# Kernel optimization log

Measured on AMD Instinct MI355X. Metric: run time of the kernel, lower is better.

Reference implementation:

```python
import jax, jax.numpy as jnp
import numpy as np

SLOPE = 0.15  # LeakyReLU negative slope used throughout the module

def leaky(v):
    return jnp.where(v >= 0, v, SLOPE * v)

def _linear_params(key, fan_in, fan_out):
    kw, kb = jax.random.split(key)
    bound = 1.0 / np.sqrt(fan_in)
    W = jax.random.uniform(kw, (fan_in, fan_out), minval=-bound, maxval=bound, dtype=jnp.float32)
    b = jax.random.uniform(kb, (fan_out,), minval=-bound, maxval=bound, dtype=jnp.float32)
    return W, b

N_NODES = 50000
N_EDGES = 640000
IN_DIM = 128
EDGE_DIM = 64
HID = 128
LAT = 64

def setup_inputs() -> dict:
    key = jax.random.key(0)
    ks = jax.random.split(key, 12)
    x = jax.random.normal(ks[0], (N_NODES, IN_DIM), dtype=jnp.float32)
    edge_index = jax.random.randint(ks[1], (2, N_EDGES), 0, N_NODES, dtype=jnp.int32)
    edge_attr = jax.random.normal(ks[2], (N_EDGES, EDGE_DIM), dtype=jnp.float32)
    # conv1 params
    e1W1, e1b1 = _linear_params(ks[3], EDGE_DIM, HID)
    e1W2, e1b2 = _linear_params(ks[4], HID, HID)
    n1W, n1b = _linear_params(ks[5], IN_DIM + HID, HID)
    # conv2 params
    e2W1, e2b1 = _linear_params(ks[6], EDGE_DIM, HID)
    e2W2, e2b2 = _linear_params(ks[7], HID, HID)
    n2W, n2b = _linear_params(ks[8], HID + HID, HID)
    muW, mub = _linear_params(ks[9], HID, LAT)
    lvW, lvb = _linear_params(ks[10], HID, LAT)
    return {"x": x, "edge_index": edge_index, "edge_attr": edge_attr,
            "e1W1": e1W1, "e1b1": e1b1, "e1W2": e1W2, "e1b2": e1b2, "n1W": n1W, "n1b": n1b,
            "e2W1": e2W1, "e2b1": e2b1, "e2W2": e2W2, "e2b2": e2b2, "n2W": n2W, "n2b": n2b,
            "muW": muW, "mub": mub, "lvW": lvW, "lvb": lvb}

def edge_encoder(x, edge_index, edge_attr, eW1, eb1, eW2, eb2, nW, nb):
    # edge MLP: Linear -> LeakyReLU(0.15) -> Linear
    emb = leaky(edge_attr @ eW1 + eb1) @ eW2 + eb2           # [E, H]
    dst = edge_index[1]                                       # PyG x_i = x[target]
    z = jnp.concatenate([x[dst], emb], axis=1)                # [E, in+H]
    msg = z @ nW + nb                                         # [E, H]
    return jax.ops.segment_sum(msg, dst, num_segments=x.shape[0])  # aggr='add'

def reference(x, edge_index, edge_attr,
              e1W1, e1b1, e1W2, e1b2, n1W, n1b,
              e2W1, e2b1, e2W2, e2b2, n2W, n2b,
              muW, mub, lvW, lvb):
    # Dropout is identity in eval mode.
    h = leaky(edge_encoder(x, edge_index, edge_attr, e1W1, e1b1, e1W2, e1b2, n1W, n1b))
    h = leaky(edge_encoder(h, edge_index, edge_attr, e2W1, e2b1, e2W2, e2b2, n2W, n2b))
    mu = h @ muW + mub
    logvar = h @ lvW + lvb
    return (mu, logvar)
```

## Files before the change

kernel.cpp:

```cpp
#include <hip/hip_runtime.h>

typedef __bf16 bf16x4 __attribute__((ext_vector_type(4)));
typedef __bf16 bf16x8 __attribute__((ext_vector_type(8)));
typedef float  f32x4  __attribute__((ext_vector_type(4)));

constexpr int N_NODES = 50000;
constexpr int N_EDGES = 640000;
constexpr int NTILES  = 98;
constexpr int NB_EDGE = 2500;

__device__ __forceinline__ float leaky(float v) { return v >= 0.f ? v : 0.15f * v; }

__global__ void prep_kernel(
    const float* __restrict__ e1W1, const float* __restrict__ e1b1,
    const float* __restrict__ e1W2, const float* __restrict__ e1b2,
    const float* __restrict__ n1W,  const float* __restrict__ n1b,
    const float* __restrict__ e2W1, const float* __restrict__ e2b1,
    const float* __restrict__ e2W2, const float* __restrict__ e2b2,
    const float* __restrict__ n2W,  const float* __restrict__ n2b,
    const float* __restrict__ muW,  const float* __restrict__ mub,
    const float* __restrict__ lvW,  const float* __restrict__ lvb,
    __bf16* __restrict__ packE, __bf16* __restrict__ packN1,
    __bf16* __restrict__ packN2, __bf16* __restrict__ packH,
    float* __restrict__ ebias, float* __restrict__ c1, float* __restrict__ c2,
    float* __restrict__ hbias)
{
    int bid = blockIdx.x;
    int lane = threadIdx.x;
    int quad = lane >> 4, low = lane & 15;

    if (bid < 32) {
        int ct = bid >> 1, kt = bid & 1;
        for (int j = 0; j < 8; ++j) {
            int k = kt * 32 + quad * 8 + j;
            int n = ct * 16 + low;
            float v = (n < 128) ? e1W1[k * 128 + n] : e2W1[k * 128 + (n - 128)];
            packE[((ct * 2 + kt) * 64 + lane) * 8 + j] = (__bf16)v;
        }
    } else if (bid < 160) {
        bool is1 = bid < 96;
        int tile = bid - (is1 ? 32 : 96);
        const float* nW  = is1 ? n1W  : n2W;
        const float* eW2 = is1 ? e1W2 : e2W2;
        __bf16* dst = is1 ? packN1 : packN2;
        int ct = tile >> 3, kt = tile & 7;
        for (int j = 0; j < 8; ++j) {
            int k = kt * 32 + quad * 8 + j;
            int n = ct * 16 + low;
            float v;
            if (k < 128) {
                v = nW[k * 128 + n];
            } else {
                int i = k - 128;
                float acc = 0.f;
                for (int k2 = 0; k2 < 128; ++k2)
                    acc += eW2[i * 128 + k2] * nW[(128 + k2) * 128 + n];
                v = acc;
            }
            dst[((ct * 8 + kt) * 64 + lane) * 8 + j] = (__bf16)v;
        }
    } else if (bid < 192) {
        int tile = bid - 160;
        int ct = tile >> 2, kt = tile & 3;
        for (int j = 0; j < 8; ++j) {
            int k = kt * 32 + quad * 8 + j;
            int n = ct * 16 + low;
            float v = (n < 64) ? muW[k * 64 + n] : lvW[k * 64 + (n - 64)];
            packH[((ct * 4 + kt) * 64 + lane) * 8 + j] = (__bf16)v;
        }
    } else if (bid == 192 || bid == 193) {
        const float* nW  = (bid == 192) ? n1W  : n2W;
        const float* nb  = (bid == 192) ? n1b  : n2b;
        const float* eb2 = (bid == 192) ? e1b2 : e2b2;
        float* dst = (bid == 192) ? c1 : c2;
        for (int rep = 0; rep < 2; ++rep) {
            int j = lane + rep * 64;
            float acc = nb[j];
            for (int k = 0; k < 128; ++k)
                acc += eb2[k] * nW[(128 + k) * 128 + j];
            dst[j] = acc;
        }
    } else {
        for (int rep = 0; rep < 4; ++rep) {
            int j = lane + rep * 64;
            ebias[j] = (j < 128) ? e1b1[j] : e2b1[j - 128];
        }
        for (int rep = 0; rep < 2; ++rep) {
            int j = lane + rep * 64;
            hbias[j] = (j < 64) ? mub[j] : lvb[j - 64];
        }
    }
}

__global__ void hist_kernel(const int* __restrict__ dstp, int* __restrict__ deg) {
    int e = blockIdx.x * 256 + threadIdx.x;
    if (e < N_EDGES) atomicAdd(&deg[dstp[e]], 1);
}

__global__ void scan_a(const int* __restrict__ deg, int* __restrict__ offs,
                       int* __restrict__ tileSum, float* __restrict__ degf) {
    __shared__ int s[512];
    int t = threadIdx.x, i = blockIdx.x * 512 + t;
    int v = (i < N_NODES) ? deg[i] : 0;
    if (i < N_NODES) degf[i] = (float)v;
    s[t] = v; __syncthreads();
    for (int off = 1; off < 512; off <<= 1) {
        int x = (t >= off) ? s[t - off] : 0;
        __syncthreads();
        s[t] += x;
        __syncthreads();
    }
    if (i < N_NODES) offs[i] = s[t] - v;
    if (t == 511) tileSum[blockIdx.x] = s[511];
}

__global__ void scan_b(const int* __restrict__ tileSum, int* __restrict__ tileOff) {
    __shared__ int s[128];
    int t = threadIdx.x;
    int v = (t < NTILES) ? tileSum[t] : 0;
    s[t] = v; __syncthreads();
    for (int off = 1; off < 128; off <<= 1) {
        int x = (t >= off) ? s[t - off] : 0;
        __syncthreads();
        s[t] += x;
        __syncthreads();
    }
    if (t < NTILES) tileOff[t] = s[t] - v;
}

__global__ void scatter_kernel(const int* __restrict__ dstp, const int* __restrict__ offs,
                               const int* __restrict__ tileOff,
                               int* __restrict__ cursor, int* __restrict__ sorted,
                               int* __restrict__ sdst) {
    int e = blockIdx.x * 256 + threadIdx.x;
    if (e < N_EDGES) {
        int d = dstp[e];
        int p = offs[d] + tileOff[d >> 9] + atomicAdd(&cursor[d], 1);
        sorted[p] = e;
        sdst[p] = d;
    }
}

__global__ __launch_bounds__(256, 3) void edge_kernel(
    const float* __restrict__ edge_attr,
    const int* __restrict__ sorted, const int* __restrict__ sdst,
    const __bf16* __restrict__ packE,
    const float* __restrict__ ebias, float* __restrict__ S)
{
    __shared__ alignas(16) __bf16 Asd[2][64 * 64];
    __shared__ alignas(16) __bf16 Lball[4][64 * 64];

    int tid = threadIdx.x;
    int w = tid >> 6, lane = tid & 63;
    int quad = lane >> 4, low = lane & 15;
    int r = tid >> 2, c0 = (tid & 3) * 16;

    auto swz = [](int row, int cb) { return row * 128 + (cb ^ ((row & 7) << 4)); };

    bf16x8 bfragE[2][4];
    #pragma unroll
    for (int kt = 0; kt < 2; ++kt)
        #pragma unroll
        for (int ct = 0; ct < 4; ++ct)
            bfragE[kt][ct] = *reinterpret_cast<const bf16x8*>(
                packE + (((w * 4 + ct) * 2 + kt) * 64 + lane) * 8);
    float bias_c[4];
    #pragma unroll
    for (int ct = 0; ct < 4; ++ct) bias_c[ct] = ebias[w * 64 + ct * 16 + low];

    char* LbB = reinterpret_cast<char*>(&Lball[w][0]);

    constexpr int STRIDE = NB_EDGE * 64;
    int e0 = blockIdx.x * 64;

    auto stage = [&](int buf, const float4& a0, const float4& a1,
                     const float4& a2, const float4& a3) {
        char* AsB = reinterpret_cast<char*>(&Asd[buf][0]);
        bf16x8 v0, v1;
        v0[0]=(__bf16)a0.x; v0[1]=(__bf16)a0.y; v0[2]=(__bf16)a0.z; v0[3]=(__bf16)a0.w;
        v0[4]=(__bf16)a1.x; v0[5]=(__bf16)a1.y; v0[6]=(__bf16)a1.z; v0[7]=(__bf16)a1.w;
        v1[0]=(__bf16)a2.x; v1[1]=(__bf16)a2.y; v1[2]=(__bf16)a2.z; v1[3]=(__bf16)a2.w;
        v1[4]=(__bf16)a3.x; v1[5]=(__bf16)a3.y; v1[6]=(__bf16)a3.z; v1[7]=(__bf16)a3.w;
        *reinterpret_cast<bf16x8*>(AsB + swz(r, c0 * 2))      = v0;
        *reinterpret_cast<bf16x8*>(AsB + swz(r, c0 * 2 + 16)) = v1;
    };

    float4 f0, f1, f2, f3;
    int md_c, md_n, md_n2, ei_n2;
    {
        int ei = sorted[e0 + r];
        md_c = sdst[e0 + lane];
        const float4* ap = reinterpret_cast<const float4*>(edge_attr + (size_t)ei * 64 + c0);
        f0 = ap[0]; f1 = ap[1]; f2 = ap[2]; f3 = ap[3];
    }
    stage(0, f0, f1, f2, f3);
    {
        int ei1 = sorted[e0 + STRIDE + r];
        md_n = sdst[e0 + STRIDE + lane];
        const float4* ap = reinterpret_cast<const float4*>(edge_attr + (size_t)ei1 * 64 + c0);
        f0 = ap[0]; f1 = ap[1]; f2 = ap[2]; f3 = ap[3];
    }
    ei_n2 = sorted[e0 + 2 * STRIDE + r];
    md_n2 = sdst[e0 + 2 * STRIDE + lane];
    __syncthreads();
    int cur = 0;

    #pragma unroll 1
    for (int it = 0; it < 4; ++it) {
        if (it < 3) stage(cur ^ 1, f0, f1, f2, f3);

        float4 g0{}, g1{}, g2{}, g3{};
        if (it < 2) {
            const float4* gp = reinterpret_cast<const float4*>(
                edge_attr + (size_t)ei_n2 * 64 + c0);
            g0 = gp[0]; g1 = gp[1]; g2 = gp[2]; g3 = gp[3];
        }
        int ei_n3 = 0, md_n3 = 0;
        if (it < 1) {
            ei_n3 = sorted[e0 + 3 * STRIDE + r];
            md_n3 = sdst[e0 + 3 * STRIDE + lane];
        }

        int dp = __shfl_up(md_c, 1);
        bool flag = (lane > 0) && (md_c != dp);
        unsigned long long mask = __ballot(flag);
        int nruns = __popcll(mask) + 1;
        int rid = __popcll(mask & ((1ull << lane) - 1ull)) + (flag ? 1 : 0);
        int vdst = __builtin_amdgcn_ds_permute(rid << 2, md_c);

        const char* AsB = reinterpret_cast<const char*>(&Asd[cur][0]);
        f32x4 C1[4][4] = {};
        #pragma unroll
        for (int kt = 0; kt < 2; ++kt)
            #pragma unroll
            for (int rt = 0; rt < 4; ++rt) {
                bf16x8 a = *reinterpret_cast<const bf16x8*>(
                    AsB + swz(rt * 16 + low, kt * 64 + quad * 16));
                #pragma unroll
                for (int ct = 0; ct < 4; ++ct)
                    C1[rt][ct] = __builtin_amdgcn_mfma_f32_16x16x32_bf16(
                        a, bfragE[kt][ct], C1[rt][ct], 0, 0, 0);
            }

        #pragma unroll
        for (int rt = 0; rt < 4; ++rt)
            #pragma unroll
            for (int ct = 0; ct < 4; ++ct) {
                bf16x4 v;
                #pragma unroll
                for (int rr = 0; rr < 4; ++rr)
                    v[rr] = (__bf16)leaky(C1[rt][ct][rr] + bias_c[ct]);
                *reinterpret_cast<bf16x4*>(
                    LbB + swz(ct * 16 + low, rt * 32 + quad * 8)) = v;
            }

        for (int rt2 = 0; rt2 * 16 < nruns; ++rt2) {
            int target = rt2 * 16 + low;
            f32x4 C2[4] = {};
            #pragma unroll
            for (int kt = 0; kt < 2; ++kt) {
                int bsh = 63 - kt * 32 - quad * 8;
                bf16x8 a;
                #pragma unroll
                for (int j = 0; j < 8; ++j) {
                    int ride = __popcll(mask << (bsh - j));
                    a[j] = (ride == target) ? (__bf16)1.0f : (__bf16)0.0f;
                }
                #pragma unroll
                for (int ct = 0; ct < 4; ++ct) {
                    bf16x8 b = *reinterpret_cast<const bf16x8*>(
                        LbB + swz(ct * 16 + low, kt * 64 + quad * 16));
                    C2[ct] = __builtin_amdgcn_mfma_f32_16x16x32_bf16(a, b, C2[ct], 0, 0, 0);
                }
            }
            int node4[4];
            #pragma unroll
            for (int rr = 0; rr < 4; ++rr)
                node4[rr] = __shfl(vdst, rt2 * 16 + quad * 4 + rr);
            #pragma unroll
            for (int ct = 0; ct < 4; ++ct) {
                int col = w * 64 + ct * 16 + low;
                #pragma unroll
                for (int rr = 0; rr < 4; ++rr) {
                    int run = rt2 * 16 + quad * 4 + rr;
                    if (run < nruns && (unsigned)node4[rr] < (unsigned)N_NODES)
                        unsafeAtomicAdd(&S[(size_t)node4[rr] * 256 + col], C2[ct][rr]);
                }
            }
        }

        if (it < 3) __syncthreads();

        f0 = g0; f1 = g1; f2 = g2; f3 = g3;
        md_c = md_n; md_n = md_n2; md_n2 = md_n3; ei_n2 = ei_n3;
        cur ^= 1;
    }
}

__global__ __launch_bounds__(256) void node_fused(
    const float* __restrict__ x, const float* __restrict__ S,
    const float* __restrict__ degf,
    const __bf16* __restrict__ packN1, const __bf16* __restrict__ packN2,
    const __bf16* __restrict__ packH,
    const float* __restrict__ c1, const float* __restrict__ c2,
    const float* __restrict__ hbias,
    float* __restrict__ out)
{
    constexpr int HS = 152;
    __shared__ __bf16 Hs[4][16 * HS];
    int w = threadIdx.x >> 6, lane = threadIdx.x & 63;
    int quad = lane >> 4, low = lane & 15;
    int rb = blockIdx.x * 64 + w * 16;

    int arow = rb + low;
    if (arow >= N_NODES) arow = N_NODES - 1;
    float ds = degf[arow];
    const float* xrow = x + (size_t)arow * 128;
    const float* Srow = S + (size_t)arow * 256;

    float deg4[4];
    #pragma unroll
    for (int rr = 0; rr < 4; ++rr) {
        int row = rb + quad * 4 + rr;
        deg4[rr] = degf[row < N_NODES ? row : N_NODES - 1];
    }

    __bf16* Hw = Hs[w];

    f32x4 C[8] = {};
    #pragma unroll
    for (int kt = 0; kt < 8; ++kt) {
        const float* base = (kt < 4) ? (xrow + kt * 32 + quad * 8)
                                     : (Srow + (kt - 4) * 32 + quad * 8);
        float4 p0 = *reinterpret_cast<const float4*>(base);
        float4 p1 = *reinterpret_cast<const float4*>(base + 4);
        float m = (kt < 4) ? ds : 1.f;
        bf16x8 a;
        a[0]=(__bf16)(p0.x*m); a[1]=(__bf16)(p0.y*m); a[2]=(__bf16)(p0.z*m); a[3]=(__bf16)(p0.w*m);
        a[4]=(__bf16)(p1.x*m); a[5]=(__bf16)(p1.y*m); a[6]=(__bf16)(p1.z*m); a[7]=(__bf16)(p1.w*m);
        #pragma unroll
        for (int ct = 0; ct < 8; ++ct) {
            bf16x8 b = *reinterpret_cast<const bf16x8*>(packN1 + ((ct * 8 + kt) * 64 + lane) * 8);
            C[ct] = __builtin_amdgcn_mfma_f32_16x16x32_bf16(a, b, C[ct], 0, 0, 0);
        }
    }
    #pragma unroll
    for (int ct = 0; ct < 8; ++ct) {
        int col = ct * 16 + low;
        float cb = c1[col];
        #pragma unroll
        for (int rr = 0; rr < 4; ++rr) {
            float v = leaky(C[ct][rr] + deg4[rr] * cb);
            Hw[(quad * 4 + rr) * HS + col] = (__bf16)(v * deg4[rr]);
        }
    }

    f32x4 C2[8] = {};
    #pragma unroll
    for (int kt = 0; kt < 8; ++kt) {
        bf16x8 a;
        if (kt < 4) {
            a = *reinterpret_cast<const bf16x8*>(&Hw[low * HS + kt * 32 + quad * 8]);
        } else {
            const float* base = Srow + 128 + (kt - 4) * 32 + quad * 8;
            float4 p0 = *reinterpret_cast<const float4*>(base);
            float4 p1 = *reinterpret_cast<const float4*>(base + 4);
            a[0]=(__bf16)p0.x; a[1]=(__bf16)p0.y; a[2]=(__bf16)p0.z; a[3]=(__bf16)p0.w;
            a[4]=(__bf16)p1.x; a[5]=(__bf16)p1.y; a[6]=(__bf16)p1.z; a[7]=(__bf16)p1.w;
        }
        #pragma unroll
        for (int ct = 0; ct < 8; ++ct) {
            bf16x8 b = *reinterpret_cast<const bf16x8*>(packN2 + ((ct * 8 + kt) * 64 + lane) * 8);
            C2[ct] = __builtin_amdgcn_mfma_f32_16x16x32_bf16(a, b, C2[ct], 0, 0, 0);
        }
    }
    #pragma unroll
    for (int ct = 0; ct < 8; ++ct) {
        int col = ct * 16 + low;
        float cb = c2[col];
        #pragma unroll
        for (int rr = 0; rr < 4; ++rr) {
            float v = leaky(C2[ct][rr] + deg4[rr] * cb);
            Hw[(quad * 4 + rr) * HS + col] = (__bf16)v;
        }
    }

    f32x4 C3[8] = {};
    #pragma unroll
    for (int kt = 0; kt < 4; ++kt) {
        bf16x8 a = *reinterpret_cast<const bf16x8*>(&Hw[low * HS + kt * 32 + quad * 8]);
        #pragma unroll
        for (int ct = 0; ct < 8; ++ct) {
            bf16x8 b = *reinterpret_cast<const bf16x8*>(packH + ((ct * 4 + kt) * 64 + lane) * 8);
            C3[ct] = __builtin_amdgcn_mfma_f32_16x16x32_bf16(a, b, C3[ct], 0, 0, 0);
        }
    }
    #pragma unroll
    for (int ct = 0; ct < 8; ++ct) {
        int col = ct * 16 + low;
        float hb = hbias[col];
        #pragma unroll
        for (int rr = 0; rr < 4; ++rr) {
            int row = rb + quad * 4 + rr;
            if (row >= N_NODES) continue;
            float v = C3[ct][rr] + hb;
            if (col < 64) out[(size_t)row * 64 + col] = v;
            else          out[(size_t)N_NODES * 64 + (size_t)row * 64 + (col - 64)] = v;
        }
    }
}

extern "C" void kernel_launch(void* const* d_in, const int* in_sizes, int n_in,
                              void* d_out, int out_size, void* d_ws, size_t ws_size,
                              hipStream_t stream)
{
    const float* x     = (const float*)d_in[0];
    const int*   eidx  = (const int*)  d_in[1];
    const float* eattr = (const float*)d_in[2];
    const float* e1W1 = (const float*)d_in[3];
    const float* e1b1 = (const float*)d_in[4];
    const float* e1W2 = (const float*)d_in[5];
    const float* e1b2 = (const float*)d_in[6];
    const float* n1W  = (const float*)d_in[7];
    const float* n1b  = (const float*)d_in[8];
    const float* e2W1 = (const float*)d_in[9];
    const float* e2b1 = (const float*)d_in[10];
    const float* e2W2 = (const float*)d_in[11];
    const float* e2b2 = (const float*)d_in[12];
    const float* n2W  = (const float*)d_in[13];
    const float* n2b  = (const float*)d_in[14];
    const float* muW  = (const float*)d_in[15];
    const float* mub  = (const float*)d_in[16];
    const float* lvW  = (const float*)d_in[17];
    const float* lvb  = (const float*)d_in[18];

    const int* dstp = eidx + N_EDGES;

    char* ws = (char*)d_ws;
    size_t off = 0;
    auto alloc = [&](size_t bytes) -> void* {
        void* p = ws + off;
        off = (off + bytes + 1023) & ~(size_t)1023;
        return p;
    };
    float* S       = (float*)alloc((size_t)N_NODES * 256 * 4);
    float* h       = (float*)alloc((size_t)N_NODES * 128 * 4);
    float* g       = (float*)alloc((size_t)N_NODES * 128 * 4);
    int*   deg     = (int*)  alloc((size_t)N_NODES * 4);
    int*   cursor  = (int*)  alloc((size_t)N_NODES * 4);
    int*   offs    = (int*)  alloc((size_t)N_NODES * 4);
    float* degf    = (float*)alloc((size_t)N_NODES * 4);
    int*   sorted  = (int*)  alloc((size_t)N_EDGES * 4);
    int*   tileSum = (int*)  alloc(NTILES * 4);
    int*   tileOff = (int*)  alloc(NTILES * 4);
    __bf16* packE  = (__bf16*)alloc(32 * 64 * 8 * 2);
    __bf16* packN1 = (__bf16*)alloc(64 * 64 * 8 * 2);
    __bf16* packN2 = (__bf16*)alloc(64 * 64 * 8 * 2);
    __bf16* packH  = (__bf16*)alloc(32 * 64 * 8 * 2);
    float* ebias   = (float*)alloc(256 * 4);
    float* c1      = (float*)alloc(128 * 4);
    float* c2      = (float*)alloc(128 * 4);
    float* hbias   = (float*)alloc(128 * 4);
    (void)ws_size; (void)in_sizes; (void)n_in; (void)out_size; (void)h;

    int* sdst = (int*)g;

    hipMemsetAsync(S, 0, (size_t)N_NODES * 256 * 4, stream);
    hipMemsetAsync(deg, 0, 2 * (((size_t)N_NODES * 4 + 1023) & ~(size_t)1023), stream);

    prep_kernel<<<195, 64, 0, stream>>>(e1W1, e1b1, e1W2, e1b2, n1W, n1b,
                                        e2W1, e2b1, e2W2, e2b2, n2W, n2b,
                                        muW, mub, lvW, lvb,
                                        packE, packN1, packN2, packH,
                                        ebias, c1, c2, hbias);

    hist_kernel<<<N_EDGES / 256, 256, 0, stream>>>(dstp, deg);
    scan_a<<<NTILES, 512, 0, stream>>>(deg, offs, tileSum, degf);
    scan_b<<<1, 128, 0, stream>>>(tileSum, tileOff);
    scatter_kernel<<<N_EDGES / 256, 256, 0, stream>>>(dstp, offs, tileOff, cursor, sorted, sdst);

    edge_kernel<<<NB_EDGE, 256, 0, stream>>>(eattr, sorted, sdst, packE, ebias, S);

    node_fused<<<(N_NODES + 63) / 64, 256, 0, stream>>>(
        x, S, degf, packN1, packN2, packH, c1, c2, hbias, (float*)d_out);
}
```

Measured before the change: 527.5 us.

## Replace persistent pipelined edge kernel with one 64-edge tile per block

```diff
diff --git a/kernel.cpp b/kernel.cpp
--- a/kernel.cpp
+++ b/kernel.cpp
@@ -7,7 +7,6 @@
 constexpr int N_NODES = 50000;
 constexpr int N_EDGES = 640000;
 constexpr int NTILES  = 98;
-constexpr int NB_EDGE = 2500;
 
 __device__ __forceinline__ float leaky(float v) { return v >= 0.f ? v : 0.15f * v; }
 
@@ -141,13 +140,13 @@
     }
 }
 
-__global__ __launch_bounds__(256, 3) void edge_kernel(
+__global__ __launch_bounds__(256, 4) void edge_kernel(
     const float* __restrict__ edge_attr,
     const int* __restrict__ sorted, const int* __restrict__ sdst,
     const __bf16* __restrict__ packE,
     const float* __restrict__ ebias, float* __restrict__ S)
 {
-    __shared__ alignas(16) __bf16 Asd[2][64 * 64];
+    __shared__ alignas(16) __bf16 As[64 * 64];
     __shared__ alignas(16) __bf16 Lball[4][64 * 64];
 
     int tid = threadIdx.x;
@@ -157,143 +156,99 @@
 
     auto swz = [](int row, int cb) { return row * 128 + (cb ^ ((row & 7) << 4)); };
 
-    bf16x8 bfragE[2][4];
-    #pragma unroll
-    for (int kt = 0; kt < 2; ++kt)
-        #pragma unroll
-        for (int ct = 0; ct < 4; ++ct)
-            bfragE[kt][ct] = *reinterpret_cast<const bf16x8*>(
-                packE + (((w * 4 + ct) * 2 + kt) * 64 + lane) * 8);
+    char* AsB = reinterpret_cast<char*>(As);
+    char* LbB = reinterpret_cast<char*>(&Lball[w][0]);
+
+    int e0 = blockIdx.x * 64;
+
+    int ei = sorted[e0 + r];
+    int md = sdst[e0 + lane];
+    const float4* ap = reinterpret_cast<const float4*>(edge_attr + (size_t)ei * 64 + c0);
+    float4 f0 = ap[0], f1 = ap[1], f2 = ap[2], f3 = ap[3];
+
+    int dp = __shfl_up(md, 1);
+    bool flag = (lane > 0) && (md != dp);
+    unsigned long long mask = __ballot(flag);
+    int nruns = __popcll(mask) + 1;
+    int rid = __popcll(mask & ((1ull << lane) - 1ull)) + (flag ? 1 : 0);
+    int vdst = __builtin_amdgcn_ds_permute(rid << 2, md);
+
     float bias_c[4];
     #pragma unroll
     for (int ct = 0; ct < 4; ++ct) bias_c[ct] = ebias[w * 64 + ct * 16 + low];
 
-    char* LbB = reinterpret_cast<char*>(&Lball[w][0]);
-
-    constexpr int STRIDE = NB_EDGE * 64;
-    int e0 = blockIdx.x * 64;
-
-    auto stage = [&](int buf, const float4& a0, const float4& a1,
-                     const float4& a2, const float4& a3) {
-        char* AsB = reinterpret_cast<char*>(&Asd[buf][0]);
+    {
         bf16x8 v0, v1;
-        v0[0]=(__bf16)a0.x; v0[1]=(__bf16)a0.y; v0[2]=(__bf16)a0.z; v0[3]=(__bf16)a0.w;
-        v0[4]=(__bf16)a1.x; v0[5]=(__bf16)a1.y; v0[6]=(__bf16)a1.z; v0[7]=(__bf16)a1.w;
-        v1[0]=(__bf16)a2.x; v1[1]=(__bf16)a2.y; v1[2]=(__bf16)a2.z; v1[3]=(__bf16)a2.w;
-        v1[4]=(__bf16)a3.x; v1[5]=(__bf16)a3.y; v1[6]=(__bf16)a3.z; v1[7]=(__bf16)a3.w;
+        v0[0]=(__bf16)f0.x; v0[1]=(__bf16)f0.y; v0[2]=(__bf16)f0.z; v0[3]=(__bf16)f0.w;
+        v0[4]=(__bf16)f1.x; v0[5]=(__bf16)f1.y; v0[6]=(__bf16)f1.z; v0[7]=(__bf16)f1.w;
+        v1[0]=(__bf16)f2.x; v1[1]=(__bf16)f2.y; v1[2]=(__bf16)f2.z; v1[3]=(__bf16)f2.w;
+        v1[4]=(__bf16)f3.x; v1[5]=(__bf16)f3.y; v1[6]=(__bf16)f3.z; v1[7]=(__bf16)f3.w;
         *reinterpret_cast<bf16x8*>(AsB + swz(r, c0 * 2))      = v0;
         *reinterpret_cast<bf16x8*>(AsB + swz(r, c0 * 2 + 16)) = v1;
-    };
-
-    float4 f0, f1, f2, f3;
-    int md_c, md_n, md_n2, ei_n2;
-    {
-        int ei = sorted[e0 + r];
-        md_c = sdst[e0 + lane];
-        const float4* ap = reinterpret_cast<const float4*>(edge_attr + (size_t)ei * 64 + c0);
-        f0 = ap[0]; f1 = ap[1]; f2 = ap[2]; f3 = ap[3];
-    }
-    stage(0, f0, f1, f2, f3);
-    {
-        int ei1 = sorted[e0 + STRIDE + r];
-        md_n = sdst[e0 + STRIDE + lane];
-        const float4* ap = reinterpret_cast<const float4*>(edge_attr + (size_t)ei1 * 64 + c0);
-        f0 = ap[0]; f1 = ap[1]; f2 = ap[2]; f3 = ap[3];
-    }
-    ei_n2 = sorted[e0 + 2 * STRIDE + r];
-    md_n2 = sdst[e0 + 2 * STRIDE + lane];
+    }
     __syncthreads();
-    int cur = 0;
-
-    #pragma unroll 1
-    for (int it = 0; it < 4; ++it) {
-        if (it < 3) stage(cur ^ 1, f0, f1, f2, f3);
-
-        float4 g0{}, g1{}, g2{}, g3{};
-        if (it < 2) {
-            const float4* gp = reinterpret_cast<const float4*>(
-                edge_attr + (size_t)ei_n2 * 64 + c0);
-            g0 = gp[0]; g1 = gp[1]; g2 = gp[2]; g3 = gp[3];
-        }
-        int ei_n3 = 0, md_n3 = 0;
-        if (it < 1) {
-            ei_n3 = sorted[e0 + 3 * STRIDE + r];
-            md_n3 = sdst[e0 + 3 * STRIDE + lane];
-        }
-
-        int dp = __shfl_up(md_c, 1);
-        bool flag = (lane > 0) && (md_c != dp);
-        unsigned long long mask = __ballot(flag);
-        int nruns = __popcll(mask) + 1;
-        int rid = __popcll(mask & ((1ull << lane) - 1ull)) + (flag ? 1 : 0);
-        int vdst = __builtin_amdgcn_ds_permute(rid << 2, md_c);
-
-        const char* AsB = reinterpret_cast<const char*>(&Asd[cur][0]);
-        f32x4 C1[4][4] = {};
-        #pragma unroll
-        for (int kt = 0; kt < 2; ++kt)
-            #pragma unroll
-            for (int rt = 0; rt < 4; ++rt) {
-                bf16x8 a = *reinterpret_cast<const bf16x8*>(
-                    AsB + swz(rt * 16 + low, kt * 64 + quad * 16));
-                #pragma unroll
-                for (int ct = 0; ct < 4; ++ct)
-                    C1[rt][ct] = __builtin_amdgcn_mfma_f32_16x16x32_bf16(
-                        a, bfragE[kt][ct], C1[rt][ct], 0, 0, 0);
-            }
-
-        #pragma unroll
-        for (int rt = 0; rt < 4; ++rt)
+
+    f32x4 C1[4][4] = {};
+    #pragma unroll
+    for (int kt = 0; kt < 2; ++kt)
+        #pragma unroll
+        for (int rt = 0; rt < 4; ++rt) {
+            bf16x8 a = *reinterpret_cast<const bf16x8*>(
+                AsB + swz(rt * 16 + low, kt * 64 + quad * 16));
             #pragma unroll
             for (int ct = 0; ct < 4; ++ct) {
-                bf16x4 v;
-                #pragma unroll
-                for (int rr = 0; rr < 4; ++rr)
-                    v[rr] = (__bf16)leaky(C1[rt][ct][rr] + bias_c[ct]);
-                *reinterpret_cast<bf16x4*>(
-                    LbB + swz(ct * 16 + low, rt * 32 + quad * 8)) = v;
+                bf16x8 b = *reinterpret_cast<const bf16x8*>(
+                    packE + (((w * 4 + ct) * 2 + kt) * 64 + lane) * 8);
+                C1[rt][ct] = __builtin_amdgcn_mfma_f32_16x16x32_bf16(
+                    a, b, C1[rt][ct], 0, 0, 0);
             }
-
-        for (int rt2 = 0; rt2 * 16 < nruns; ++rt2) {
-            int target = rt2 * 16 + low;
-            f32x4 C2[4] = {};
-            #pragma unroll
-            for (int kt = 0; kt < 2; ++kt) {
-                int bsh = 63 - kt * 32 - quad * 8;
-                bf16x8 a;
-                #pragma unroll
-                for (int j = 0; j < 8; ++j) {
-                    int ride = __popcll(mask << (bsh - j));
-                    a[j] = (ride == target) ? (__bf16)1.0f : (__bf16)0.0f;
-                }
-                #pragma unroll
-                for (int ct = 0; ct < 4; ++ct) {
-                    bf16x8 b = *reinterpret_cast<const bf16x8*>(
-                        LbB + swz(ct * 16 + low, kt * 64 + quad * 16));
-                    C2[ct] = __builtin_amdgcn_mfma_f32_16x16x32_bf16(a, b, C2[ct], 0, 0, 0);
-                }
-            }
-            int node4[4];
+        }
+
+    #pragma unroll
+    for (int rt = 0; rt < 4; ++rt)
+        #pragma unroll
+        for (int ct = 0; ct < 4; ++ct) {
+            bf16x4 v;
             #pragma unroll
             for (int rr = 0; rr < 4; ++rr)
-                node4[rr] = __shfl(vdst, rt2 * 16 + quad * 4 + rr);
+                v[rr] = (__bf16)leaky(C1[rt][ct][rr] + bias_c[ct]);
+            *reinterpret_cast<bf16x4*>(
+                LbB + swz(ct * 16 + low, rt * 32 + quad * 8)) = v;
+        }
+
+    for (int rt2 = 0; rt2 * 16 < nruns; ++rt2) {
+        int target = rt2 * 16 + low;
+        f32x4 C2[4] = {};
+        #pragma unroll
+        for (int kt = 0; kt < 2; ++kt) {
+            int bsh = 63 - kt * 32 - quad * 8;
+            bf16x8 a;
+            #pragma unroll
+            for (int j = 0; j < 8; ++j) {
+                int ride = __popcll(mask << (bsh - j));
+                a[j] = (ride == target) ? (__bf16)1.0f : (__bf16)0.0f;
+            }
             #pragma unroll
             for (int ct = 0; ct < 4; ++ct) {
-                int col = w * 64 + ct * 16 + low;
-                #pragma unroll
-                for (int rr = 0; rr < 4; ++rr) {
-                    int run = rt2 * 16 + quad * 4 + rr;
-                    if (run < nruns && (unsigned)node4[rr] < (unsigned)N_NODES)
-                        unsafeAtomicAdd(&S[(size_t)node4[rr] * 256 + col], C2[ct][rr]);
-                }
+                bf16x8 b = *reinterpret_cast<const bf16x8*>(
+                    LbB + swz(ct * 16 + low, kt * 64 + quad * 16));
+                C2[ct] = __builtin_amdgcn_mfma_f32_16x16x32_bf16(a, b, C2[ct], 0, 0, 0);
             }
         }
-
-        if (it < 3) __syncthreads();
-
-        f0 = g0; f1 = g1; f2 = g2; f3 = g3;
-        md_c = md_n; md_n = md_n2; md_n2 = md_n3; ei_n2 = ei_n3;
-        cur ^= 1;
+        int node4[4];
+        #pragma unroll
+        for (int rr = 0; rr < 4; ++rr)
+            node4[rr] = __shfl(vdst, rt2 * 16 + quad * 4 + rr);
+        #pragma unroll
+        for (int ct = 0; ct < 4; ++ct) {
+            int col = w * 64 + ct * 16 + low;
+            #pragma unroll
+            for (int rr = 0; rr < 4; ++rr) {
+                int run = rt2 * 16 + quad * 4 + rr;
+                if (run < nruns && (unsigned)node4[rr] < (unsigned)N_NODES)
+                    unsafeAtomicAdd(&S[(size_t)node4[rr] * 256 + col], C2[ct][rr]);
+            }
+        }
     }
 }
 
@@ -479,7 +434,7 @@
     scan_b<<<1, 128, 0, stream>>>(tileSum, tileOff);
     scatter_kernel<<<N_EDGES / 256, 256, 0, stream>>>(dstp, offs, tileOff, cursor, sorted, sdst);
 
-    edge_kernel<<<NB_EDGE, 256, 0, stream>>>(eattr, sorted, sdst, packE, ebias, S);
+    edge_kernel<<<N_EDGES / 64, 256, 0, stream>>>(eattr, sorted, sdst, packE, ebias, S);
 
     node_fused<<<(N_NODES + 63) / 64, 256, 0, stream>>>(
         x, S, degf, packN1, packN2, packH, c1, c2, hbias, (float*)d_out);
```

Measured after the change: 456.1 us. 13.5% less time.
